# Kernel optimization log

Hardware: AMD Instinct MI355X
Metric: run time of the kernel (lower is better)

Reference implementation:

```python
import jax, jax.numpy as jnp
import numpy as np

N, T, S, E, H, DFF = 4, 2048, 2048, 512, 8, 2048
DH = E // H
EPS = 1e-5


def layer_norm(x, w, b):
    m = jnp.mean(x, axis=-1, keepdims=True)
    v = jnp.mean(jnp.square(x - m), axis=-1, keepdims=True)
    return (x - m) * jax.lax.rsqrt(v + EPS) * w + b


def mha(q, k, v, wq, bq, wk, bk, wv, bv, wo, bo, mask=None):
    # q: (N,Tq,E), k/v: (N,Tk,E); torch Linear convention: y = x @ W.T + b
    Nq, Tq, _ = q.shape
    Tk = k.shape[1]
    Q = (q @ wq.T + bq).reshape(Nq, Tq, H, DH).transpose(0, 2, 1, 3)  # (N,H,Tq,DH)
    K = (k @ wk.T + bk).reshape(Nq, Tk, H, DH).transpose(0, 2, 1, 3)
    V = (v @ wv.T + bv).reshape(Nq, Tk, H, DH).transpose(0, 2, 1, 3)
    scores = jnp.einsum('bhtd,bhsd->bhts', Q, K) * (1.0 / np.sqrt(DH))  # (N,H,Tq,Tk)
    if mask is not None:
        scores = jnp.where(mask, scores, jnp.float32(-1e9))
    attn = jax.nn.softmax(scores, axis=-1)
    out = jnp.einsum('bhts,bhsd->bhtd', attn, V)  # (N,H,Tq,DH)
    out = out.transpose(0, 2, 1, 3).reshape(Nq, Tq, E)
    return out @ wo.T + bo


def setup_inputs() -> dict:
    key = jax.random.key(0)
    ks = jax.random.split(key, 20)
    s = 0.02

    def lin(k, out_d, in_d):
        return jax.random.normal(k, (out_d, in_d), jnp.float32) * s

    inp = {
        'tgt': jax.random.normal(ks[0], (N, T, E), jnp.float32),
        'memory': jax.random.normal(ks[1], (N, S, E), jnp.float32),
        'tgt_mask': jnp.tril(jnp.ones((T, T), dtype=bool)),  # causal (T,T)
        # self-attention params
        'sa_wq': lin(ks[2], E, E), 'sa_bq': jnp.zeros((E,), jnp.float32),
        'sa_wk': lin(ks[3], E, E), 'sa_bk': jnp.zeros((E,), jnp.float32),
        'sa_wv': lin(ks[4], E, E), 'sa_bv': jnp.zeros((E,), jnp.float32),
        'sa_wo': lin(ks[5], E, E), 'sa_bo': jnp.zeros((E,), jnp.float32),
        # cross-attention params
        'ca_wq': lin(ks[6], E, E), 'ca_bq': jnp.zeros((E,), jnp.float32),
        'ca_wk': lin(ks[7], E, E), 'ca_bk': jnp.zeros((E,), jnp.float32),
        'ca_wv': lin(ks[8], E, E), 'ca_bv': jnp.zeros((E,), jnp.float32),
        'ca_wo': lin(ks[9], E, E), 'ca_bo': jnp.zeros((E,), jnp.float32),
        # FFN params
        'w1': lin(ks[10], DFF, E), 'b1': jnp.zeros((DFF,), jnp.float32),
        'w2': lin(ks[11], E, DFF), 'b2': jnp.zeros((E,), jnp.float32),
        # LayerNorm params
        'ln1_w': jnp.ones((E,), jnp.float32), 'ln1_b': jnp.zeros((E,), jnp.float32),
        'ln2_w': jnp.ones((E,), jnp.float32), 'ln2_b': jnp.zeros((E,), jnp.float32),
        'ln3_w': jnp.ones((E,), jnp.float32), 'ln3_b': jnp.zeros((E,), jnp.float32),
    }
    return inp


def reference(tgt, memory, tgt_mask,
              sa_wq, sa_bq, sa_wk, sa_bk, sa_wv, sa_bv, sa_wo, sa_bo,
              ca_wq, ca_bq, ca_wk, ca_bk, ca_wv, ca_bv, ca_wo, ca_bo,
              w1, b1, w2, b2,
              ln1_w, ln1_b, ln2_w, ln2_b, ln3_w, ln3_b):
    # stage 1: masked self-attention + residual + LN (dropout=0 / eval mode)
    sa = mha(tgt, tgt, tgt, sa_wq, sa_bq, sa_wk, sa_bk, sa_wv, sa_bv, sa_wo, sa_bo, mask=tgt_mask)
    x = layer_norm(tgt + sa, ln1_w, ln1_b)
    # stage 2: cross-attention over encoder memory + residual + LN
    ca = mha(x, memory, memory, ca_wq, ca_bq, ca_wk, ca_bk, ca_wv, ca_bv, ca_wo, ca_bo)
    x = layer_norm(x + ca, ln2_w, ln2_b)
    # stage 3: FFN (ReLU) + residual + LN
    mlp = jax.nn.relu(x @ w1.T + b1) @ w2.T + b2
    out = layer_norm(x + mlp, ln3_w, ln3_b)
    return out
```

## Files before the change

### kernel.cpp

```cpp
#include <hip/hip_runtime.h>
#include <hip/hip_bf16.h>
#include <cstdint>

typedef short short8 __attribute__((ext_vector_type(8)));
typedef short short4v __attribute__((ext_vector_type(4)));
typedef float f32x4 __attribute__((ext_vector_type(4)));
typedef float f32x16 __attribute__((ext_vector_type(16)));

#define GLL16(gp, lp) __builtin_amdgcn_global_load_lds( \
    (const __attribute__((address_space(1))) unsigned int*)(gp), \
    (__attribute__((address_space(3))) unsigned int*)(lp), 16, 0, 0)
#define WAITV(n) asm volatile("s_waitcnt vmcnt(" #n ")" ::: "memory")

__device__ __forceinline__ float bf2f(ushort u) {
    union { unsigned int i; float f; } v; v.i = ((unsigned int)u) << 16; return v.f;
}
__device__ __forceinline__ ushort f2bf(float f) {
    union { float f; unsigned int u; } v; v.f = f;
    unsigned int r = v.u + 0x7FFFu + ((v.u >> 16) & 1u);
    return (ushort)(r >> 16);
}
__device__ __forceinline__ int cvtpk_bf16(float lo, float hi) {
    int r;
    asm("v_cvt_pk_bf16_f32 %0, %1, %2" : "=v"(r) : "v"(lo), "v"(hi));
    return r;
}
__device__ __forceinline__ void plane32_swap(int& a, int& b) {
    asm volatile("v_permlane32_swap_b32 %0, %1" : "+v"(a), "+v"(b));
}
__device__ __forceinline__ float fast_exp2(float x) {
    float r;
    asm("v_exp_f32 %0, %1" : "=v"(r) : "v"(x));
    return r;
}

#define SCQ 0.18033688f

struct CvtArgs {
    const float* src[12];
    ushort*      dst[12];
};
__global__ __launch_bounds__(256) void f2b_all(CvtArgs a)
{
    int id = blockIdx.x;
    int seg, boff;
    if (id < 4096)       { seg = 0; boff = id; }
    else if (id < 8192)  { seg = 1; boff = id - 4096; }
    else if (id < 10240) { int t = id - 8192; seg = 2 + (t >> 8); boff = t & 255; }
    else if (id < 11264) { seg = 10; boff = id - 10240; }
    else                 { seg = 11; boff = id - 11264; }
    int i = (boff * 256 + threadIdx.x) * 4;
    f32x4 v = *(const f32x4*)(a.src[seg] + i);
    short4v o;
#pragma unroll
    for (int e = 0; e < 4; ++e) o[e] = (short)f2bf(v[e]);
    *(short4v*)(a.dst[seg] + i) = o;
}

template<int MODE, int DEPTH, int TN>
__global__ __launch_bounds__(256) void gemm_bt(
    const ushort* __restrict__ A, const ushort* __restrict__ W,
    const float* __restrict__ b0, const float* __restrict__ b1,
    const float* __restrict__ b2,
    ushort* __restrict__ C0, ushort* __restrict__ C1, ushort* __restrict__ C2,
    int M, int N, int K)
{
    constexpr int NI = TN / 32;
    constexpr int L  = (TN == 128) ? 4 : 3;
    __shared__ ushort As[DEPTH][128 * 32];
    __shared__ ushort Bs[DEPTH][TN * 32];
    const int tid = threadIdx.x;
    const int l  = tid & 63;
    const int w  = tid >> 6;
    const int wr = w >> 1, wc = w & 1;
    const int bn = blockIdx.x, bm = blockIdx.y;
    const int lg = l >> 4, li = l & 15;

    const ushort* Ab = A + (size_t)(bm * 128) * K;
    const ushort* Bb = W + (size_t)(bn * TN) * K;

    f32x4 acc[4][NI] = {};

    const int r0 = tid >> 2,         s0 = (tid & 3) ^ ((r0 >> 2) & 3);
    const int r1 = (tid + 256) >> 2, s1 = (tid & 3) ^ ((r1 >> 2) & 3);

    auto stage = [&](int buf, int kt) {
        const ushort* Ak = Ab + kt * 32;
        const ushort* Bk = Bb + kt * 32;
        GLL16(Ak + (size_t)r0 * K + s0 * 8, &As[buf][tid * 8]);
        GLL16(Ak + (size_t)r1 * K + s1 * 8, &As[buf][(tid + 256) * 8]);
        GLL16(Bk + (size_t)r0 * K + s0 * 8, &Bs[buf][tid * 8]);
        if (TN == 128)
            GLL16(Bk + (size_t)r1 * K + s1 * 8, &Bs[buf][(tid + 256) * 8]);
    };

    const int nk = K >> 5;
#pragma unroll
    for (int p = 0; p < DEPTH - 1; ++p)
        if (p < nk) stage(p, p);

    for (int kt = 0; kt < nk; ++kt) {
        const int b = kt & (DEPTH - 1);
        const int nxt = kt + DEPTH - 1;
        if (nxt < nk) stage(nxt & (DEPTH - 1), nxt);
        const int rem = nk - 1 - kt;
        const int fl = rem < DEPTH - 1 ? rem : DEPTH - 1;
        if (L == 4) {
            if (fl >= 3)      WAITV(12);
            else if (fl == 2) WAITV(8);
            else if (fl == 1) WAITV(4);
            else              WAITV(0);
        } else {
            if (fl >= 3)      WAITV(9);
            else if (fl == 2) WAITV(6);
            else if (fl == 1) WAITV(3);
            else              WAITV(0);
        }
        __builtin_amdgcn_s_barrier();
        __builtin_amdgcn_sched_barrier(0);

        short8 af[4], bfr[NI];
#pragma unroll
        for (int mi = 0; mi < 4; ++mi) {
            int row = wr * 64 + mi * 16 + li;
            int ch  = lg ^ ((row >> 2) & 3);
            af[mi] = *(const short8*)(&As[b][row * 32 + ch * 8]);
        }
#pragma unroll
        for (int ni = 0; ni < NI; ++ni) {
            int row = wc * (TN / 2) + ni * 16 + li;
            int ch  = lg ^ ((row >> 2) & 3);
            bfr[ni] = *(const short8*)(&Bs[b][row * 32 + ch * 8]);
        }
#pragma unroll
        for (int mi = 0; mi < 4; ++mi)
#pragma unroll
            for (int ni = 0; ni < NI; ++ni)
                acc[mi][ni] = __builtin_amdgcn_mfma_f32_16x16x32_bf16(
                    af[mi], bfr[ni], acc[mi][ni], 0, 0, 0);

        __builtin_amdgcn_sched_barrier(0);
        asm volatile("s_waitcnt lgkmcnt(0)" ::: "memory");
        __builtin_amdgcn_s_barrier();
    }

    const int crow0 = bm * 128 + wr * 64 + lg * 4;
    const int ccol0 = bn * TN + wc * (TN / 2) + li;
    const int sec = (MODE == 2 || MODE == 3) ? (bn >> 2) : 0;
    const float* bp = b0;
    ushort* Cw = C0;
    bool vsec = false;
    if (MODE == 2) {
        bp = (sec == 0) ? b0 : (sec == 1) ? b1 : b2;
        Cw = (sec == 0) ? C0 : (sec == 1) ? C1 : C2;
        vsec = (sec == 2);
    } else if (MODE == 3) {
        bp = (sec == 0) ? b0 : b1;
        Cw = (sec == 0) ? C0 : C1;
        vsec = (sec == 1);
    }
    const int Nout = (MODE == 2 || MODE == 3) ? 512 : N;
    const float scl = (MODE == 4 || (MODE == 2 && sec == 0)) ? SCQ : 1.f;

#pragma unroll
    for (int ni = 0; ni < NI; ++ni) {
        int col = ccol0 + ni * 16;
        int cl  = (MODE == 2 || MODE == 3) ? (col & 511) : col;
        float bv = bp[cl];
#pragma unroll
        for (int mi = 0; mi < 4; ++mi) {
            int row = crow0 + mi * 16;
            if (vsec) {
                int n = row >> 11, t = row & 2047;
                int h = cl >> 6,  d = cl & 63;
                size_t base = ((size_t)((n * 8 + h) * 64 + d)) * 2048 + t;
                short4v pk;
#pragma unroll
                for (int r = 0; r < 4; ++r) pk[r] = (short)f2bf(acc[mi][ni][r] + bv);
                *(short4v*)(Cw + base) = pk;
            } else {
#pragma unroll
                for (int r = 0; r < 4; ++r) {
                    float v = (acc[mi][ni][r] + bv) * scl;
                    if (MODE == 1) v = fmaxf(v, 0.f);
                    Cw[(size_t)(row + r) * Nout + cl] = f2bf(v);
                }
            }
        }
    }
}

template<bool CAUSAL>
__global__ __launch_bounds__(256) void attn_kernel(
    const ushort* __restrict__ Q, const ushort* __restrict__ K,
    const ushort* __restrict__ Vt, ushort* __restrict__ P0,
    ushort* __restrict__ P1, float* __restrict__ Ls, int Tk)
{
    __shared__ ushort SH[16384];
    const int tid = threadIdx.x;
    const int l = tid & 63, wq = tid >> 6;
    const int c = l & 31, hi = l >> 5;

    int qt, nh, ck;
    if (CAUSAL) {
        int g = (int)blockIdx.x >> 6;
        qt = (g < 8) ? (15 - g) : (g - 8);
        int r = blockIdx.x & 63;
        nh = r >> 1; ck = r & 1;
    } else {
        int pos = ((int)blockIdx.x & 7) * 128 + ((int)blockIdx.x >> 3);
        nh = pos >> 5; ck = (pos >> 4) & 1; qt = pos & 15;
    }
    const int q0 = qt * 128;
    const int n = nh >> 3, h = nh & 7;
    const int qrow = q0 + wq * 32 + c;

    short8 qf[4];
#pragma unroll
    for (int s = 0; s < 4; ++s)
        qf[s] = *(const short8*)(Q + (size_t)(n * 2048 + qrow) * 512
                                   + h * 64 + s * 16 + hi * 8);

    f32x16 oacc[2] = {};
    f32x16 oS = {};
    const short ONE = (short)0x3F80;
    const short8 ones = {ONE, ONE, ONE, ONE, ONE, ONE, ONE, ONE};

    const ushort* Kbase = K + (size_t)(n * 2048) * 512 + h * 64;
    const ushort* Vbase = Vt + (size_t)nh * 64 * Tk;

    const int rowA = tid >> 3;
    const int csA  = (tid & 7) ^ (rowA & 7);

    auto stage = [&](int buf, int j0) {
        ushort* kd = SH + buf * 4096;
        ushort* vd = SH + 8192 + buf * 4096;
        GLL16(Kbase + (size_t)(j0 + rowA) * 512 + csA * 8,      kd + tid * 8);
        GLL16(Kbase + (size_t)(j0 + rowA + 32) * 512 + csA * 8, kd + (tid + 256) * 8);
        GLL16(Vbase + (size_t)rowA * Tk + j0 + csA * 8,         vd + tid * 8);
        GLL16(Vbase + (size_t)(rowA + 32) * Tk + j0 + csA * 8,  vd + (tid + 256) * 8);
    };

    const int cnt = CAUSAL ? (qt + 1) : (Tk >> 7);

    stage(0, ck * 64);
    for (int s = 0; s < cnt; ++s) {
        const int b  = s & 1;
        const int j0 = (ck + 2 * s) << 6;
        if (s + 1 < cnt) {
            stage(b ^ 1, j0 + 128);
            WAITV(4);
        } else {
            WAITV(0);
        }
        __builtin_amdgcn_s_barrier();
        __builtin_amdgcn_sched_barrier(0);

        const ushort* kls = SH + b * 4096;
        const ushort* vls = SH + 8192 + b * 4096;

        f32x16 sacc[2] = {};
        __builtin_amdgcn_s_setprio(1);
#pragma unroll
        for (int ks = 0; ks < 4; ++ks) {
#pragma unroll
            for (int t2 = 0; t2 < 2; ++t2) {
                int row = t2 * 32 + c;
                int ch  = (ks * 2 + hi) ^ (row & 7);
                short8 kf = *(const short8*)(kls + row * 64 + ch * 8);
                sacc[t2] = __builtin_amdgcn_mfma_f32_32x32x16_bf16(
                    kf, qf[ks], sacc[t2], 0, 0, 0);
            }
        }
        __builtin_amdgcn_s_setprio(0);

        const bool domask = CAUSAL && (j0 + 64 > q0);
#pragma unroll
        for (int t2 = 0; t2 < 2; ++t2) {
            float pv[16];
#pragma unroll
            for (int reg = 0; reg < 16; ++reg) {
                float p = fast_exp2(sacc[t2][reg]);
                if (domask) {
                    int jg = j0 + t2 * 32 + (reg & 3) + 8 * (reg >> 2) + 4 * hi;
                    if (jg > qrow) p = 0.f;
                }
                pv[reg] = p;
            }
            int X0 = cvtpk_bf16(pv[0],  pv[1]),  Y0 = cvtpk_bf16(pv[2],  pv[3]);
            int X1 = cvtpk_bf16(pv[4],  pv[5]),  Y1 = cvtpk_bf16(pv[6],  pv[7]);
            int X2 = cvtpk_bf16(pv[8],  pv[9]),  Y2 = cvtpk_bf16(pv[10], pv[11]);
            int X3 = cvtpk_bf16(pv[12], pv[13]), Y3 = cvtpk_bf16(pv[14], pv[15]);
            plane32_swap(X0, X1); plane32_swap(Y0, Y1);
            plane32_swap(X2, X3); plane32_swap(Y2, Y3);
            union { int i[4]; short8 s; } pa0 = {{X0, Y0, X1, Y1}},
                                          pa1 = {{X2, Y2, X3, Y3}};
            __builtin_amdgcn_s_setprio(1);
            oS = __builtin_amdgcn_mfma_f32_32x32x16_bf16(pa0.s, ones, oS, 0, 0, 0);
            oS = __builtin_amdgcn_mfma_f32_32x32x16_bf16(pa1.s, ones, oS, 0, 0, 0);
#pragma unroll
            for (int sp = 0; sp < 2; ++sp) {
                short8 pa = sp ? pa1.s : pa0.s;
#pragma unroll
                for (int dc = 0; dc < 2; ++dc) {
                    int row = dc * 32 + c;
                    int ch  = (t2 * 4 + sp * 2 + hi) ^ (row & 7);
                    short8 vb = *(const short8*)(vls + row * 64 + ch * 8);
                    oacc[dc] = __builtin_amdgcn_mfma_f32_32x32x16_bf16(
                        pa, vb, oacc[dc], 0, 0, 0);
                }
            }
            __builtin_amdgcn_s_setprio(0);
        }

        __builtin_amdgcn_sched_barrier(0);
        asm volatile("s_waitcnt lgkmcnt(0)" ::: "memory");
        __builtin_amdgcn_s_barrier();
    }

    ushort* Pw = ck ? P1 : P0;
    if (c == 0) {
#pragma unroll
        for (int reg = 0; reg < 16; ++reg) {
            int qloc = (reg & 3) + 8 * (reg >> 2) + 4 * hi;
            Ls[ck * 65536 + nh * 2048 + q0 + wq * 32 + qloc] = oS[reg];
        }
    }
#pragma unroll
    for (int dc = 0; dc < 2; ++dc)
#pragma unroll
        for (int reg = 0; reg < 16; ++reg) {
            int qloc = (reg & 3) + 8 * (reg >> 2) + 4 * hi;
            size_t off = (size_t)(n * 2048 + q0 + wq * 32 + qloc) * 512
                       + h * 64 + dc * 32 + c;
            Pw[off] = f2bf(oacc[dc][reg]);
        }
}

__global__ __launch_bounds__(256) void attn_merge(
    const ushort* __restrict__ P0, const ushort* __restrict__ P1,
    const float* __restrict__ Ls, ushort* __restrict__ out)
{
    const int row = blockIdx.x * 4 + (threadIdx.x >> 6);
    const int l = threadIdx.x & 63;
    const size_t off = (size_t)row * 512 + l * 8;
    const int n = row >> 11, q = row & 2047, h = l >> 3;
    const int lidx = (n * 8 + h) * 2048 + q;
    float linv = 1.f / (Ls[lidx] + Ls[65536 + lidx]);
    short8 a = *(const short8*)(P0 + off);
    short8 b = *(const short8*)(P1 + off);
    short8 o;
#pragma unroll
    for (int e = 0; e < 8; ++e)
        o[e] = (short)f2bf((bf2f((ushort)a[e]) + bf2f((ushort)b[e])) * linv);
    *(short8*)(out + off) = o;
}

template<int F32OUT>
__global__ __launch_bounds__(256) void ln_kernel(
    const ushort* __restrict__ X, const ushort* __restrict__ Y,
    const float* __restrict__ W, const float* __restrict__ B,
    void* __restrict__ outp)
{
    const int row = blockIdx.x * 4 + (threadIdx.x >> 6);
    const int l = threadIdx.x & 63;
    const size_t off = (size_t)row * 512 + l * 8;
    short8 xv = *(const short8*)(X + off);
    short8 yv = *(const short8*)(Y + off);
    float v[8], s = 0.f, s2 = 0.f;
#pragma unroll
    for (int e = 0; e < 8; ++e) {
        float f = bf2f((ushort)xv[e]) + bf2f((ushort)yv[e]);
        v[e] = f; s += f; s2 += f * f;
    }
#pragma unroll
    for (int m = 1; m < 64; m <<= 1) {
        s  += __shfl_xor(s,  m);
        s2 += __shfl_xor(s2, m);
    }
    float mean = s * (1.f / 512.f);
    float var  = s2 * (1.f / 512.f) - mean * mean;
    float rs   = rsqrtf(var + 1e-5f);
    f32x4 w0 = *(const f32x4*)(W + l * 8);
    f32x4 w1 = *(const f32x4*)(W + l * 8 + 4);
    f32x4 b0 = *(const f32x4*)(B + l * 8);
    f32x4 b1 = *(const f32x4*)(B + l * 8 + 4);
    float wv[8] = {w0[0], w0[1], w0[2], w0[3], w1[0], w1[1], w1[2], w1[3]};
    float bv[8] = {b0[0], b0[1], b0[2], b0[3], b1[0], b1[1], b1[2], b1[3]};
    if (F32OUT) {
        float* out = (float*)outp;
#pragma unroll
        for (int e = 0; e < 8; ++e)
            out[off + e] = (v[e] - mean) * rs * wv[e] + bv[e];
    } else {
        ushort* out = (ushort*)outp;
        short8 ov;
#pragma unroll
        for (int e = 0; e < 8; ++e)
            ov[e] = (short)f2bf((v[e] - mean) * rs * wv[e] + bv[e]);
        *(short8*)(out + off) = ov;
    }
}

extern "C" void kernel_launch(void* const* d_in, const int* in_sizes, int n_in,
                              void* d_out, int out_size, void* d_ws, size_t ws_size,
                              hipStream_t stream)
{
    (void)in_sizes; (void)n_in; (void)out_size; (void)ws_size;
    const float* tgt  = (const float*)d_in[0];
    const float* mem  = (const float*)d_in[1];
    const float* sa_wq = (const float*)d_in[3];
    const float* sa_bq = (const float*)d_in[4];
    const float* sa_wk = (const float*)d_in[5];
    const float* sa_bk = (const float*)d_in[6];
    const float* sa_wv = (const float*)d_in[7];
    const float* sa_bv = (const float*)d_in[8];
    const float* sa_wo = (const float*)d_in[9];
    const float* sa_bo = (const float*)d_in[10];
    const float* ca_wq = (const float*)d_in[11];
    const float* ca_bq = (const float*)d_in[12];
    const float* ca_wk = (const float*)d_in[13];
    const float* ca_bk = (const float*)d_in[14];
    const float* ca_wv = (const float*)d_in[15];
    const float* ca_bv = (const float*)d_in[16];
    const float* ca_wo = (const float*)d_in[17];
    const float* ca_bo = (const float*)d_in[18];
    const float* w1    = (const float*)d_in[19];
    const float* b1    = (const float*)d_in[20];
    const float* w2    = (const float*)d_in[21];
    const float* b2    = (const float*)d_in[22];
    const float* ln1w  = (const float*)d_in[23];
    const float* ln1b  = (const float*)d_in[24];
    const float* ln2w  = (const float*)d_in[25];
    const float* ln2b  = (const float*)d_in[26];
    const float* ln3w  = (const float*)d_in[27];
    const float* ln3b  = (const float*)d_in[28];

    const size_t SE = (size_t)8192 * 512;
    const size_t EE = (size_t)512 * 512;
    ushort* ws = (ushort*)d_ws;
    ushort* Wb   = ws;
    ushort* bsqkv = Wb;
    ushort* bswo  = Wb + 3 * EE;
    ushort* bcwq  = Wb + 4 * EE;
    ushort* bckv  = Wb + 5 * EE;
    ushort* bcwo  = Wb + 7 * EE;
    ushort* bw1   = Wb + 8 * EE;
    ushort* bw2   = bw1 + 4 * EE;
    ushort* tgtb = Wb + 16 * EE;
    ushort* memb = tgtb + SE;
    ushort* Qb   = memb + SE;
    ushort* Kb   = Qb + SE;
    ushort* Vb   = Kb + SE;
    ushort* X1   = Vb + SE;
    ushort* AO   = X1 + SE;
    float*  LsBuf = (float*)(AO + SE);
    ushort* PO   = Qb;
    ushort* X2   = tgtb;
    ushort* Hb   = Qb;

    dim3 blk(256);
    dim3 gqkv(12, 64);
    dim3 gkv(8, 64);
    dim3 g64n(8, 64);
    dim3 g2048(16, 64);
    dim3 ga(1024);
    dim3 gln(2048);

    CvtArgs ca;
    ca.src[0] = tgt;    ca.dst[0] = tgtb;
    ca.src[1] = mem;    ca.dst[1] = memb;
    ca.src[2] = sa_wq;  ca.dst[2] = bsqkv;
    ca.src[3] = sa_wk;  ca.dst[3] = bsqkv + EE;
    ca.src[4] = sa_wv;  ca.dst[4] = bsqkv + 2 * EE;
    ca.src[5] = sa_wo;  ca.dst[5] = bswo;
    ca.src[6] = ca_wq;  ca.dst[6] = bcwq;
    ca.src[7] = ca_wk;  ca.dst[7] = bckv;
    ca.src[8] = ca_wv;  ca.dst[8] = bckv + EE;
    ca.src[9] = ca_wo;  ca.dst[9] = bcwo;
    ca.src[10] = w1;    ca.dst[10] = bw1;
    ca.src[11] = w2;    ca.dst[11] = bw2;
    f2b_all<<<12288, blk, 0, stream>>>(ca);

    gemm_bt<2, 2, 128><<<gqkv, blk, 0, stream>>>(tgtb, bsqkv, sa_bq, sa_bk, sa_bv,
                                                 Qb, Kb, Vb, 8192, 1536, 512);
    attn_kernel<true><<<ga, blk, 0, stream>>>(Qb, Kb, Vb, AO, X1, LsBuf, 2048);
    attn_merge<<<gln, blk, 0, stream>>>(AO, X1, LsBuf, AO);
    gemm_bt<0, 4, 64><<<g64n, blk, 0, stream>>>(AO, bswo, sa_bo, nullptr, nullptr,
                                                PO, nullptr, nullptr, 8192, 512, 512);
    ln_kernel<0><<<gln, blk, 0, stream>>>(tgtb, PO, ln1w, ln1b, X1);

    gemm_bt<4, 4, 64><<<g64n, blk, 0, stream>>>(X1, bcwq, ca_bq, nullptr, nullptr,
                                                Qb, nullptr, nullptr, 8192, 512, 512);
    gemm_bt<3, 2, 128><<<gkv, blk, 0, stream>>>(memb, bckv, ca_bk, ca_bv, nullptr,
                                                Kb, Vb, nullptr, 8192, 1024, 512);
    attn_kernel<false><<<ga, blk, 0, stream>>>(Qb, Kb, Vb, AO, tgtb, LsBuf, 2048);
    attn_merge<<<gln, blk, 0, stream>>>(AO, tgtb, LsBuf, AO);
    gemm_bt<0, 4, 64><<<g64n, blk, 0, stream>>>(AO, bcwo, ca_bo, nullptr, nullptr,
                                                PO, nullptr, nullptr, 8192, 512, 512);
    ln_kernel<0><<<gln, blk, 0, stream>>>(X1, PO, ln2w, ln2b, X2);

    gemm_bt<1, 2, 128><<<g2048, blk, 0, stream>>>(X2, bw1, b1, nullptr, nullptr,
                                                  Hb, nullptr, nullptr, 8192, 2048, 512);
    gemm_bt<0, 4, 64><<<g64n, blk, 0, stream>>>(Hb, bw2, b2, nullptr, nullptr,
                                                AO, nullptr, nullptr, 8192, 512, 2048);
    ln_kernel<1><<<gln, blk, 0, stream>>>(X2, AO, ln3w, ln3b, d_out);
}
```

Measured before the change: 284.8 us.

## Double attention query tile per block to 256 rows, halving K/V staging

Each attention block now handles 256 query rows (64 per wave, split into two 32-row chunks) instead of 128. Each K/V tile staged into LDS is reused across twice as many queries, and the grid shrinks from 1024 to 512 blocks. In the causal case, waves skip key tiles that lie entirely beyond their rows. The cost is more registers per wave (two sets of accumulators and Q fragments), fewer blocks in flight, and more causal imbalance since waves in one block finish at different points.

Result: slower. 302.4 us (+6.2%).

```diff
diff --git a/kernel.cpp b/kernel.cpp
--- a/kernel.cpp
+++ b/kernel.cpp
@@ -204,25 +204,27 @@
     int qt, nh, ck;
     if (CAUSAL) {
         int g = (int)blockIdx.x >> 6;
-        qt = (g < 8) ? (15 - g) : (g - 8);
+        qt = (g < 4) ? (7 - g) : (g - 4);
         int r = blockIdx.x & 63;
         nh = r >> 1; ck = r & 1;
     } else {
-        int pos = ((int)blockIdx.x & 7) * 128 + ((int)blockIdx.x >> 3);
-        nh = pos >> 5; ck = (pos >> 4) & 1; qt = pos & 15;
-    }
-    const int q0 = qt * 128;
+        int pos = ((int)blockIdx.x & 7) * 64 + ((int)blockIdx.x >> 3);
+        nh = pos >> 4; ck = (pos >> 3) & 1; qt = pos & 7;
+    }
+    const int q0 = qt * 256;
     const int n = nh >> 3, h = nh & 7;
-    const int qrow = q0 + wq * 32 + c;
-
-    short8 qf[4];
-#pragma unroll
-    for (int s = 0; s < 4; ++s)
-        qf[s] = *(const short8*)(Q + (size_t)(n * 2048 + qrow) * 512
-                                   + h * 64 + s * 16 + hi * 8);
-
-    f32x16 oacc[2] = {};
-    f32x16 oS = {};
+    const int qw = q0 + wq * 64;
+
+    short8 qf[2][4];
+#pragma unroll
+    for (int ic = 0; ic < 2; ++ic)
+#pragma unroll
+        for (int s = 0; s < 4; ++s)
+            qf[ic][s] = *(const short8*)(Q + (size_t)(n * 2048 + qw + ic * 32 + c) * 512
+                                           + h * 64 + s * 16 + hi * 8);
+
+    f32x16 oacc[2][2] = {};
+    f32x16 oS[2] = {};
     const short ONE = (short)0x3F80;
     const short8 ones = {ONE, ONE, ONE, ONE, ONE, ONE, ONE, ONE};
 
@@ -241,7 +243,7 @@
         GLL16(Vbase + (size_t)(rowA + 32) * Tk + j0 + csA * 8,  vd + (tid + 256) * 8);
     };
 
-    const int cnt = CAUSAL ? (qt + 1) : (Tk >> 7);
+    const int cnt = CAUSAL ? 2 * (qt + 1) : (Tk >> 7);
 
     stage(0, ck * 64);
     for (int s = 0; s < cnt; ++s) {
@@ -256,61 +258,74 @@
         __builtin_amdgcn_s_barrier();
         __builtin_amdgcn_sched_barrier(0);
 
-        const ushort* kls = SH + b * 4096;
-        const ushort* vls = SH + 8192 + b * 4096;
-
-        f32x16 sacc[2] = {};
-        __builtin_amdgcn_s_setprio(1);
-#pragma unroll
-        for (int ks = 0; ks < 4; ++ks) {
+        const bool active = !CAUSAL || (j0 < qw + 64);
+        if (active) {
+            const ushort* kls = SH + b * 4096;
+            const ushort* vls = SH + 8192 + b * 4096;
+            const bool domask = CAUSAL && (j0 + 64 > qw);
+
 #pragma unroll
             for (int t2 = 0; t2 < 2; ++t2) {
-                int row = t2 * 32 + c;
-                int ch  = (ks * 2 + hi) ^ (row & 7);
-                short8 kf = *(const short8*)(kls + row * 64 + ch * 8);
-                sacc[t2] = __builtin_amdgcn_mfma_f32_32x32x16_bf16(
-                    kf, qf[ks], sacc[t2], 0, 0, 0);
+                f32x16 sacc[2] = {};
+                __builtin_amdgcn_s_setprio(1);
+#pragma unroll
+                for (int ks = 0; ks < 4; ++ks) {
+                    int row = t2 * 32 + c;
+                    int ch  = (ks * 2 + hi) ^ (row & 7);
+                    short8 kf = *(const short8*)(kls + row * 64 + ch * 8);
+                    sacc[0] = __builtin_amdgcn_mfma_f32_32x32x16_bf16(
+                        kf, qf[0][ks], sacc[0], 0, 0, 0);
+                    sacc[1] = __builtin_amdgcn_mfma_f32_32x32x16_bf16(
+                        kf, qf[1][ks], sacc[1], 0, 0, 0);
+                }
+                __builtin_amdgcn_s_setprio(0);
+
+                short8 pa[2][2];
+#pragma unroll
+                for (int ic = 0; ic < 2; ++ic) {
+                    const int qrow = qw + ic * 32 + c;
+                    float pv[16];
+#pragma unroll
+                    for (int reg = 0; reg < 16; ++reg) {
+                        float p = fast_exp2(sacc[ic][reg]);
+                        if (domask) {
+                            int jg = j0 + t2 * 32 + (reg & 3) + 8 * (reg >> 2) + 4 * hi;
+                            if (jg > qrow) p = 0.f;
+                        }
+                        pv[reg] = p;
+                    }
+                    int X0 = cvtpk_bf16(pv[0],  pv[1]),  Y0 = cvtpk_bf16(pv[2],  pv[3]);
+                    int X1 = cvtpk_bf16(pv[4],  pv[5]),  Y1 = cvtpk_bf16(pv[6],  pv[7]);
+                    int X2 = cvtpk_bf16(pv[8],  pv[9]),  Y2 = cvtpk_bf16(pv[10], pv[11]);
+                    int X3 = cvtpk_bf16(pv[12], pv[13]), Y3 = cvtpk_bf16(pv[14], pv[15]);
+                    plane32_swap(X0, X1); plane32_swap(Y0, Y1);
+                    plane32_swap(X2, X3); plane32_swap(Y2, Y3);
+                    union { int i[4]; short8 s; } u0 = {{X0, Y0, X1, Y1}},
+                                                  u1 = {{X2, Y2, X3, Y3}};
+                    pa[ic][0] = u0.s;
+                    pa[ic][1] = u1.s;
+                }
+
+                __builtin_amdgcn_s_setprio(1);
+                oS[0] = __builtin_amdgcn_mfma_f32_32x32x16_bf16(pa[0][0], ones, oS[0], 0, 0, 0);
+                oS[0] = __builtin_amdgcn_mfma_f32_32x32x16_bf16(pa[0][1], ones, oS[0], 0, 0, 0);
+                oS[1] = __builtin_amdgcn_mfma_f32_32x32x16_bf16(pa[1][0], ones, oS[1], 0, 0, 0);
+                oS[1] = __builtin_amdgcn_mfma_f32_32x32x16_bf16(pa[1][1], ones, oS[1], 0, 0, 0);
+#pragma unroll
+                for (int sp = 0; sp < 2; ++sp) {
+#pragma unroll
+                    for (int dc = 0; dc < 2; ++dc) {
+                        int row = dc * 32 + c;
+                        int ch  = (t2 * 4 + sp * 2 + hi) ^ (row & 7);
+                        short8 vb = *(const short8*)(vls + row * 64 + ch * 8);
+                        oacc[0][dc] = __builtin_amdgcn_mfma_f32_32x32x16_bf16(
+                            pa[0][sp], vb, oacc[0][dc], 0, 0, 0);
+                        oacc[1][dc] = __builtin_amdgcn_mfma_f32_32x32x16_bf16(
+                            pa[1][sp], vb, oacc[1][dc], 0, 0, 0);
+                    }
+                }
+                __builtin_amdgcn_s_setprio(0);
             }
-        }
-        __builtin_amdgcn_s_setprio(0);
-
-        const bool domask = CAUSAL && (j0 + 64 > q0);
-#pragma unroll
-        for (int t2 = 0; t2 < 2; ++t2) {
-            float pv[16];
-#pragma unroll
-            for (int reg = 0; reg < 16; ++reg) {
-                float p = fast_exp2(sacc[t2][reg]);
-                if (domask) {
-                    int jg = j0 + t2 * 32 + (reg & 3) + 8 * (reg >> 2) + 4 * hi;
-                    if (jg > qrow) p = 0.f;
-                }
-                pv[reg] = p;
-            }
-            int X0 = cvtpk_bf16(pv[0],  pv[1]),  Y0 = cvtpk_bf16(pv[2],  pv[3]);
-            int X1 = cvtpk_bf16(pv[4],  pv[5]),  Y1 = cvtpk_bf16(pv[6],  pv[7]);
-            int X2 = cvtpk_bf16(pv[8],  pv[9]),  Y2 = cvtpk_bf16(pv[10], pv[11]);
-            int X3 = cvtpk_bf16(pv[12], pv[13]), Y3 = cvtpk_bf16(pv[14], pv[15]);
-            plane32_swap(X0, X1); plane32_swap(Y0, Y1);
-            plane32_swap(X2, X3); plane32_swap(Y2, Y3);
-            union { int i[4]; short8 s; } pa0 = {{X0, Y0, X1, Y1}},
-                                          pa1 = {{X2, Y2, X3, Y3}};
-            __builtin_amdgcn_s_setprio(1);
-            oS = __builtin_amdgcn_mfma_f32_32x32x16_bf16(pa0.s, ones, oS, 0, 0, 0);
-            oS = __builtin_amdgcn_mfma_f32_32x32x16_bf16(pa1.s, ones, oS, 0, 0, 0);
-#pragma unroll
-            for (int sp = 0; sp < 2; ++sp) {
-                short8 pa = sp ? pa1.s : pa0.s;
-#pragma unroll
-                for (int dc = 0; dc < 2; ++dc) {
-                    int row = dc * 32 + c;
-                    int ch  = (t2 * 4 + sp * 2 + hi) ^ (row & 7);
-                    short8 vb = *(const short8*)(vls + row * 64 + ch * 8);
-                    oacc[dc] = __builtin_amdgcn_mfma_f32_32x32x16_bf16(
-                        pa, vb, oacc[dc], 0, 0, 0);
-                }
-            }
-            __builtin_amdgcn_s_setprio(0);
         }
 
         __builtin_amdgcn_sched_barrier(0);
@@ -321,20 +336,24 @@
     ushort* Pw = ck ? P1 : P0;
     if (c == 0) {
 #pragma unroll
-        for (int reg = 0; reg < 16; ++reg) {
-            int qloc = (reg & 3) + 8 * (reg >> 2) + 4 * hi;
-            Ls[ck * 65536 + nh * 2048 + q0 + wq * 32 + qloc] = oS[reg];
-        }
-    }
-#pragma unroll
-    for (int dc = 0; dc < 2; ++dc)
-#pragma unroll
-        for (int reg = 0; reg < 16; ++reg) {
-            int qloc = (reg & 3) + 8 * (reg >> 2) + 4 * hi;
-            size_t off = (size_t)(n * 2048 + q0 + wq * 32 + qloc) * 512
-                       + h * 64 + dc * 32 + c;
-            Pw[off] = f2bf(oacc[dc][reg]);
-        }
+        for (int ic = 0; ic < 2; ++ic)
+#pragma unroll
+            for (int reg = 0; reg < 16; ++reg) {
+                int qloc = (reg & 3) + 8 * (reg >> 2) + 4 * hi;
+                Ls[ck * 65536 + nh * 2048 + qw + ic * 32 + qloc] = oS[ic][reg];
+            }
+    }
+#pragma unroll
+    for (int ic = 0; ic < 2; ++ic)
+#pragma unroll
+        for (int dc = 0; dc < 2; ++dc)
+#pragma unroll
+            for (int reg = 0; reg < 16; ++reg) {
+                int qloc = (reg & 3) + 8 * (reg >> 2) + 4 * hi;
+                size_t off = (size_t)(n * 2048 + qw + ic * 32 + qloc) * 512
+                           + h * 64 + dc * 32 + c;
+                Pw[off] = f2bf(oacc[ic][dc][reg]);
+            }
 }
 
 __global__ __launch_bounds__(256) void attn_merge(
@@ -464,7 +483,7 @@
     dim3 gkv(8, 64);
     dim3 g64n(8, 64);
     dim3 g2048(16, 64);
-    dim3 ga(1024);
+    dim3 ga(512);
     dim3 gln(2048);
 
     CvtArgs ca;
```

## Split attention key dimension four ways and skip fully masked key tiles per wave

Applied to the files above, without the earlier changes.

The attention kernel now splits each query tile's key range into four interleaved chunks instead of two, doubling the grid to 2048 blocks. Each block writes its own partial output and row-sum buffer, and the merge kernel combines four partials. Within causal tiles, waves whose query rows lie entirely before a key block skip that block's compute, cutting wasted masked work. The cost is more partial-output memory traffic in the merge, an extra workspace region, and a shorter per-block loop that pipelines less.

Result: slower. 298.3 us (+4.7%).

```diff
diff --git a/kernel.cpp b/kernel.cpp
--- a/kernel.cpp
+++ b/kernel.cpp
@@ -194,7 +194,8 @@
 __global__ __launch_bounds__(256) void attn_kernel(
     const ushort* __restrict__ Q, const ushort* __restrict__ K,
     const ushort* __restrict__ Vt, ushort* __restrict__ P0,
-    ushort* __restrict__ P1, float* __restrict__ Ls, int Tk)
+    ushort* __restrict__ P1, ushort* __restrict__ P2, ushort* __restrict__ P3,
+    float* __restrict__ Ls, int Tk)
 {
     __shared__ ushort SH[16384];
     const int tid = threadIdx.x;
@@ -203,17 +204,18 @@
 
     int qt, nh, ck;
     if (CAUSAL) {
-        int g = (int)blockIdx.x >> 6;
+        int g = (int)blockIdx.x >> 7;
         qt = (g < 8) ? (15 - g) : (g - 8);
-        int r = blockIdx.x & 63;
-        nh = r >> 1; ck = r & 1;
+        int r = blockIdx.x & 127;
+        nh = r >> 2; ck = r & 3;
     } else {
-        int pos = ((int)blockIdx.x & 7) * 128 + ((int)blockIdx.x >> 3);
-        nh = pos >> 5; ck = (pos >> 4) & 1; qt = pos & 15;
+        int pos = ((int)blockIdx.x & 7) * 256 + ((int)blockIdx.x >> 3);
+        nh = pos >> 6; ck = (pos >> 4) & 3; qt = pos & 15;
     }
     const int q0 = qt * 128;
     const int n = nh >> 3, h = nh & 7;
-    const int qrow = q0 + wq * 32 + c;
+    const int qw = q0 + wq * 32;
+    const int qrow = qw + c;
 
     short8 qf[4];
 #pragma unroll
@@ -241,14 +243,14 @@
         GLL16(Vbase + (size_t)(rowA + 32) * Tk + j0 + csA * 8,  vd + (tid + 256) * 8);
     };
 
-    const int cnt = CAUSAL ? (qt + 1) : (Tk >> 7);
-
-    stage(0, ck * 64);
+    const int cnt = CAUSAL ? ((2 * qt + 5 - ck) >> 2) : (Tk >> 8);
+
+    if (cnt > 0) stage(0, ck * 64);
     for (int s = 0; s < cnt; ++s) {
         const int b  = s & 1;
-        const int j0 = (ck + 2 * s) << 6;
+        const int j0 = (ck + 4 * s) << 6;
         if (s + 1 < cnt) {
-            stage(b ^ 1, j0 + 128);
+            stage(b ^ 1, j0 + 256);
             WAITV(4);
         } else {
             WAITV(0);
@@ -256,74 +258,78 @@
         __builtin_amdgcn_s_barrier();
         __builtin_amdgcn_sched_barrier(0);
 
-        const ushort* kls = SH + b * 4096;
-        const ushort* vls = SH + 8192 + b * 4096;
-
-        f32x16 sacc[2] = {};
-        __builtin_amdgcn_s_setprio(1);
-#pragma unroll
-        for (int ks = 0; ks < 4; ++ks) {
-#pragma unroll
-            for (int t2 = 0; t2 < 2; ++t2) {
-                int row = t2 * 32 + c;
-                int ch  = (ks * 2 + hi) ^ (row & 7);
-                short8 kf = *(const short8*)(kls + row * 64 + ch * 8);
-                sacc[t2] = __builtin_amdgcn_mfma_f32_32x32x16_bf16(
-                    kf, qf[ks], sacc[t2], 0, 0, 0);
-            }
-        }
-        __builtin_amdgcn_s_setprio(0);
-
-        const bool domask = CAUSAL && (j0 + 64 > q0);
-#pragma unroll
-        for (int t2 = 0; t2 < 2; ++t2) {
-            float pv[16];
-#pragma unroll
-            for (int reg = 0; reg < 16; ++reg) {
-                float p = fast_exp2(sacc[t2][reg]);
-                if (domask) {
-                    int jg = j0 + t2 * 32 + (reg & 3) + 8 * (reg >> 2) + 4 * hi;
-                    if (jg > qrow) p = 0.f;
-                }
-                pv[reg] = p;
-            }
-            int X0 = cvtpk_bf16(pv[0],  pv[1]),  Y0 = cvtpk_bf16(pv[2],  pv[3]);
-            int X1 = cvtpk_bf16(pv[4],  pv[5]),  Y1 = cvtpk_bf16(pv[6],  pv[7]);
-            int X2 = cvtpk_bf16(pv[8],  pv[9]),  Y2 = cvtpk_bf16(pv[10], pv[11]);
-            int X3 = cvtpk_bf16(pv[12], pv[13]), Y3 = cvtpk_bf16(pv[14], pv[15]);
-            plane32_swap(X0, X1); plane32_swap(Y0, Y1);
-            plane32_swap(X2, X3); plane32_swap(Y2, Y3);
-            union { int i[4]; short8 s; } pa0 = {{X0, Y0, X1, Y1}},
-                                          pa1 = {{X2, Y2, X3, Y3}};
+        const bool active = !CAUSAL || (j0 < qw + 32);
+        if (active) {
+            const ushort* kls = SH + b * 4096;
+            const ushort* vls = SH + 8192 + b * 4096;
+            const bool domask = CAUSAL && (j0 + 64 > qw);
+
+            f32x16 sacc[2] = {};
             __builtin_amdgcn_s_setprio(1);
-            oS = __builtin_amdgcn_mfma_f32_32x32x16_bf16(pa0.s, ones, oS, 0, 0, 0);
-            oS = __builtin_amdgcn_mfma_f32_32x32x16_bf16(pa1.s, ones, oS, 0, 0, 0);
-#pragma unroll
-            for (int sp = 0; sp < 2; ++sp) {
-                short8 pa = sp ? pa1.s : pa0.s;
-#pragma unroll
-                for (int dc = 0; dc < 2; ++dc) {
-                    int row = dc * 32 + c;
-                    int ch  = (t2 * 4 + sp * 2 + hi) ^ (row & 7);
-                    short8 vb = *(const short8*)(vls + row * 64 + ch * 8);
-                    oacc[dc] = __builtin_amdgcn_mfma_f32_32x32x16_bf16(
-                        pa, vb, oacc[dc], 0, 0, 0);
+#pragma unroll
+            for (int ks = 0; ks < 4; ++ks) {
+#pragma unroll
+                for (int t2 = 0; t2 < 2; ++t2) {
+                    int row = t2 * 32 + c;
+                    int ch  = (ks * 2 + hi) ^ (row & 7);
+                    short8 kf = *(const short8*)(kls + row * 64 + ch * 8);
+                    sacc[t2] = __builtin_amdgcn_mfma_f32_32x32x16_bf16(
+                        kf, qf[ks], sacc[t2], 0, 0, 0);
                 }
             }
             __builtin_amdgcn_s_setprio(0);
+
+#pragma unroll
+            for (int t2 = 0; t2 < 2; ++t2) {
+                float pv[16];
+#pragma unroll
+                for (int reg = 0; reg < 16; ++reg) {
+                    float p = fast_exp2(sacc[t2][reg]);
+                    if (domask) {
+                        int jg = j0 + t2 * 32 + (reg & 3) + 8 * (reg >> 2) + 4 * hi;
+                        if (jg > qrow) p = 0.f;
+                    }
+                    pv[reg] = p;
+                }
+                int X0 = cvtpk_bf16(pv[0],  pv[1]),  Y0 = cvtpk_bf16(pv[2],  pv[3]);
+                int X1 = cvtpk_bf16(pv[4],  pv[5]),  Y1 = cvtpk_bf16(pv[6],  pv[7]);
+                int X2 = cvtpk_bf16(pv[8],  pv[9]),  Y2 = cvtpk_bf16(pv[10], pv[11]);
+                int X3 = cvtpk_bf16(pv[12], pv[13]), Y3 = cvtpk_bf16(pv[14], pv[15]);
+                plane32_swap(X0, X1); plane32_swap(Y0, Y1);
+                plane32_swap(X2, X3); plane32_swap(Y2, Y3);
+                union { int i[4]; short8 s; } pa0 = {{X0, Y0, X1, Y1}},
+                                              pa1 = {{X2, Y2, X3, Y3}};
+                __builtin_amdgcn_s_setprio(1);
+                oS = __builtin_amdgcn_mfma_f32_32x32x16_bf16(pa0.s, ones, oS, 0, 0, 0);
+                oS = __builtin_amdgcn_mfma_f32_32x32x16_bf16(pa1.s, ones, oS, 0, 0, 0);
+#pragma unroll
+                for (int sp = 0; sp < 2; ++sp) {
+                    short8 pa = sp ? pa1.s : pa0.s;
+#pragma unroll
+                    for (int dc = 0; dc < 2; ++dc) {
+                        int row = dc * 32 + c;
+                        int ch  = (t2 * 4 + sp * 2 + hi) ^ (row & 7);
+                        short8 vb = *(const short8*)(vls + row * 64 + ch * 8);
+                        oacc[dc] = __builtin_amdgcn_mfma_f32_32x32x16_bf16(
+                            pa, vb, oacc[dc], 0, 0, 0);
+                    }
+                }
+                __builtin_amdgcn_s_setprio(0);
+            }
         }
 
         __builtin_amdgcn_sched_barrier(0);
         asm volatile("s_waitcnt lgkmcnt(0)" ::: "memory");
         __builtin_amdgcn_s_barrier();
     }
-
-    ushort* Pw = ck ? P1 : P0;
+    WAITV(0);
+
+    ushort* Pw = (ck == 0) ? P0 : (ck == 1) ? P1 : (ck == 2) ? P2 : P3;
     if (c == 0) {
 #pragma unroll
         for (int reg = 0; reg < 16; ++reg) {
             int qloc = (reg & 3) + 8 * (reg >> 2) + 4 * hi;
-            Ls[ck * 65536 + nh * 2048 + q0 + wq * 32 + qloc] = oS[reg];
+            Ls[ck * 65536 + nh * 2048 + qw + qloc] = oS[reg];
         }
     }
 #pragma unroll
@@ -331,7 +337,7 @@
 #pragma unroll
         for (int reg = 0; reg < 16; ++reg) {
             int qloc = (reg & 3) + 8 * (reg >> 2) + 4 * hi;
-            size_t off = (size_t)(n * 2048 + q0 + wq * 32 + qloc) * 512
+            size_t off = (size_t)(n * 2048 + qw + qloc) * 512
                        + h * 64 + dc * 32 + c;
             Pw[off] = f2bf(oacc[dc][reg]);
         }
@@ -339,6 +345,7 @@
 
 __global__ __launch_bounds__(256) void attn_merge(
     const ushort* __restrict__ P0, const ushort* __restrict__ P1,
+    const ushort* __restrict__ P2, const ushort* __restrict__ P3,
     const float* __restrict__ Ls, ushort* __restrict__ out)
 {
     const int row = blockIdx.x * 4 + (threadIdx.x >> 6);
@@ -346,13 +353,19 @@
     const size_t off = (size_t)row * 512 + l * 8;
     const int n = row >> 11, q = row & 2047, h = l >> 3;
     const int lidx = (n * 8 + h) * 2048 + q;
-    float linv = 1.f / (Ls[lidx] + Ls[65536 + lidx]);
+    float linv = 1.f / (Ls[lidx] + Ls[65536 + lidx]
+                      + Ls[131072 + lidx] + Ls[196608 + lidx]);
     short8 a = *(const short8*)(P0 + off);
     short8 b = *(const short8*)(P1 + off);
+    short8 cc = *(const short8*)(P2 + off);
+    short8 d = *(const short8*)(P3 + off);
     short8 o;
 #pragma unroll
-    for (int e = 0; e < 8; ++e)
-        o[e] = (short)f2bf((bf2f((ushort)a[e]) + bf2f((ushort)b[e])) * linv);
+    for (int e = 0; e < 8; ++e) {
+        float s = bf2f((ushort)a[e]) + bf2f((ushort)b[e])
+                + bf2f((ushort)cc[e]) + bf2f((ushort)d[e]);
+        o[e] = (short)f2bf(s * linv);
+    }
     *(short8*)(out + off) = o;
 }
 
@@ -455,6 +468,8 @@
     ushort* X1   = Vb + SE;
     ushort* AO   = X1 + SE;
     float*  LsBuf = (float*)(AO + SE);
+    ushort* P2   = (ushort*)(LsBuf + 4 * 65536);
+    ushort* P3   = P2 + SE;
     ushort* PO   = Qb;
     ushort* X2   = tgtb;
     ushort* Hb   = Qb;
@@ -464,7 +479,7 @@
     dim3 gkv(8, 64);
     dim3 g64n(8, 64);
     dim3 g2048(16, 64);
-    dim3 ga(1024);
+    dim3 ga(2048);
     dim3 gln(2048);
 
     CvtArgs ca;
@@ -484,8 +499,9 @@
 
     gemm_bt<2, 2, 128><<<gqkv, blk, 0, stream>>>(tgtb, bsqkv, sa_bq, sa_bk, sa_bv,
                                                  Qb, Kb, Vb, 8192, 1536, 512);
-    attn_kernel<true><<<ga, blk, 0, stream>>>(Qb, Kb, Vb, AO, X1, LsBuf, 2048);
-    attn_merge<<<gln, blk, 0, stream>>>(AO, X1, LsBuf, AO);
+    attn_kernel<true><<<ga, blk, 0, stream>>>(Qb, Kb, Vb, AO, X1, P2, P3,
+                                              LsBuf, 2048);
+    attn_merge<<<gln, blk, 0, stream>>>(AO, X1, P2, P3, LsBuf, AO);
     gemm_bt<0, 4, 64><<<g64n, blk, 0, stream>>>(AO, bswo, sa_bo, nullptr, nullptr,
                                                 PO, nullptr, nullptr, 8192, 512, 512);
     ln_kernel<0><<<gln, blk, 0, stream>>>(tgtb, PO, ln1w, ln1b, X1);
@@ -494,8 +510,9 @@
                                                 Qb, nullptr, nullptr, 8192, 512, 512);
     gemm_bt<3, 2, 128><<<gkv, blk, 0, stream>>>(memb, bckv, ca_bk, ca_bv, nullptr,
                                                 Kb, Vb, nullptr, 8192, 1024, 512);
-    attn_kernel<false><<<ga, blk, 0, stream>>>(Qb, Kb, Vb, AO, tgtb, LsBuf, 2048);
-    attn_merge<<<gln, blk, 0, stream>>>(AO, tgtb, LsBuf, AO);
+    attn_kernel<false><<<ga, blk, 0, stream>>>(Qb, Kb, Vb, AO, tgtb, P2, P3,
+                                               LsBuf, 2048);
+    attn_merge<<<gln, blk, 0, stream>>>(AO, tgtb, P2, P3, LsBuf, AO);
     gemm_bt<0, 4, 64><<<g64n, blk, 0, stream>>>(AO, bcwo, ca_bo, nullptr, nullptr,
                                                 PO, nullptr, nullptr, 8192, 512, 512);
     ln_kernel<0><<<gln, blk, 0, stream>>>(X1, PO, ln2w, ln2b, X2);
```

## Split KV range contiguously, skip fully masked wave tiles, rotate LDS swizzle

Applied to the files above, without the earlier changes.

The two key-chunk halves are now contiguous ranges of 64-wide KV tiles split evenly, instead of interleaved 64-tile strides. This balances causal work between the two splits. Each wave skips the QK/PV compute for tiles entirely above its 32-row causal band, and the mask check is narrowed to per-wave rows. The LDS swizzle adds a row-group rotation to reduce bank conflicts in the K/V fragment reads. A trailing vmcnt wait is added for safety. The risk is wave divergence at barriers, and skipped waves still wait on the shared loads.

Result: slower. 295.6 us, median of 2 (+3.8%).

```diff
diff --git a/kernel.cpp b/kernel.cpp
--- a/kernel.cpp
+++ b/kernel.cpp
@@ -213,7 +213,8 @@
     }
     const int q0 = qt * 128;
     const int n = nh >> 3, h = nh & 7;
-    const int qrow = q0 + wq * 32 + c;
+    const int qw = q0 + wq * 32;
+    const int qrow = qw + c;
 
     short8 qf[4];
 #pragma unroll
@@ -230,25 +231,28 @@
     const ushort* Vbase = Vt + (size_t)nh * 64 * Tk;
 
     const int rowA = tid >> 3;
-    const int csA  = (tid & 7) ^ (rowA & 7);
+    const int cs0 = (((tid & 7) - (rowA >> 3)) & 7) ^ (rowA & 7);
+    const int cs1 = (((tid & 7) - (rowA >> 3) + 4) & 7) ^ (rowA & 7);
 
     auto stage = [&](int buf, int j0) {
         ushort* kd = SH + buf * 4096;
         ushort* vd = SH + 8192 + buf * 4096;
-        GLL16(Kbase + (size_t)(j0 + rowA) * 512 + csA * 8,      kd + tid * 8);
-        GLL16(Kbase + (size_t)(j0 + rowA + 32) * 512 + csA * 8, kd + (tid + 256) * 8);
-        GLL16(Vbase + (size_t)rowA * Tk + j0 + csA * 8,         vd + tid * 8);
-        GLL16(Vbase + (size_t)(rowA + 32) * Tk + j0 + csA * 8,  vd + (tid + 256) * 8);
+        GLL16(Kbase + (size_t)(j0 + rowA) * 512 + cs0 * 8,      kd + tid * 8);
+        GLL16(Kbase + (size_t)(j0 + rowA + 32) * 512 + cs1 * 8, kd + (tid + 256) * 8);
+        GLL16(Vbase + (size_t)rowA * Tk + j0 + cs0 * 8,         vd + tid * 8);
+        GLL16(Vbase + (size_t)(rowA + 32) * Tk + j0 + cs1 * 8,  vd + (tid + 256) * 8);
     };
 
-    const int cnt = CAUSAL ? (qt + 1) : (Tk >> 7);
-
-    stage(0, ck * 64);
+    const int total = CAUSAL ? (2 * qt + 2) : (Tk >> 6);
+    const int start = (ck * total) >> 1;
+    const int cnt   = (((ck + 1) * total) >> 1) - start;
+
+    if (cnt > 0) stage(0, start << 6);
     for (int s = 0; s < cnt; ++s) {
         const int b  = s & 1;
-        const int j0 = (ck + 2 * s) << 6;
+        const int j0 = (start + s) << 6;
         if (s + 1 < cnt) {
-            stage(b ^ 1, j0 + 128);
+            stage(b ^ 1, j0 + 64);
             WAITV(4);
         } else {
             WAITV(0);
@@ -256,74 +260,78 @@
         __builtin_amdgcn_s_barrier();
         __builtin_amdgcn_sched_barrier(0);
 
-        const ushort* kls = SH + b * 4096;
-        const ushort* vls = SH + 8192 + b * 4096;
-
-        f32x16 sacc[2] = {};
-        __builtin_amdgcn_s_setprio(1);
-#pragma unroll
-        for (int ks = 0; ks < 4; ++ks) {
-#pragma unroll
-            for (int t2 = 0; t2 < 2; ++t2) {
-                int row = t2 * 32 + c;
-                int ch  = (ks * 2 + hi) ^ (row & 7);
-                short8 kf = *(const short8*)(kls + row * 64 + ch * 8);
-                sacc[t2] = __builtin_amdgcn_mfma_f32_32x32x16_bf16(
-                    kf, qf[ks], sacc[t2], 0, 0, 0);
-            }
-        }
-        __builtin_amdgcn_s_setprio(0);
-
-        const bool domask = CAUSAL && (j0 + 64 > q0);
-#pragma unroll
-        for (int t2 = 0; t2 < 2; ++t2) {
-            float pv[16];
-#pragma unroll
-            for (int reg = 0; reg < 16; ++reg) {
-                float p = fast_exp2(sacc[t2][reg]);
-                if (domask) {
-                    int jg = j0 + t2 * 32 + (reg & 3) + 8 * (reg >> 2) + 4 * hi;
-                    if (jg > qrow) p = 0.f;
-                }
-                pv[reg] = p;
-            }
-            int X0 = cvtpk_bf16(pv[0],  pv[1]),  Y0 = cvtpk_bf16(pv[2],  pv[3]);
-            int X1 = cvtpk_bf16(pv[4],  pv[5]),  Y1 = cvtpk_bf16(pv[6],  pv[7]);
-            int X2 = cvtpk_bf16(pv[8],  pv[9]),  Y2 = cvtpk_bf16(pv[10], pv[11]);
-            int X3 = cvtpk_bf16(pv[12], pv[13]), Y3 = cvtpk_bf16(pv[14], pv[15]);
-            plane32_swap(X0, X1); plane32_swap(Y0, Y1);
-            plane32_swap(X2, X3); plane32_swap(Y2, Y3);
-            union { int i[4]; short8 s; } pa0 = {{X0, Y0, X1, Y1}},
-                                          pa1 = {{X2, Y2, X3, Y3}};
+        const bool active = !CAUSAL || (j0 < qw + 32);
+        if (active) {
+            const ushort* kls = SH + b * 4096;
+            const ushort* vls = SH + 8192 + b * 4096;
+            const bool domask = CAUSAL && (j0 + 64 > qw);
+
+            f32x16 sacc[2] = {};
             __builtin_amdgcn_s_setprio(1);
-            oS = __builtin_amdgcn_mfma_f32_32x32x16_bf16(pa0.s, ones, oS, 0, 0, 0);
-            oS = __builtin_amdgcn_mfma_f32_32x32x16_bf16(pa1.s, ones, oS, 0, 0, 0);
-#pragma unroll
-            for (int sp = 0; sp < 2; ++sp) {
-                short8 pa = sp ? pa1.s : pa0.s;
-#pragma unroll
-                for (int dc = 0; dc < 2; ++dc) {
-                    int row = dc * 32 + c;
-                    int ch  = (t2 * 4 + sp * 2 + hi) ^ (row & 7);
-                    short8 vb = *(const short8*)(vls + row * 64 + ch * 8);
-                    oacc[dc] = __builtin_amdgcn_mfma_f32_32x32x16_bf16(
-                        pa, vb, oacc[dc], 0, 0, 0);
+#pragma unroll
+            for (int ks = 0; ks < 4; ++ks) {
+#pragma unroll
+                for (int t2 = 0; t2 < 2; ++t2) {
+                    int row = t2 * 32 + c;
+                    int ch  = (((ks * 2 + hi) ^ (row & 7)) + (row >> 3)) & 7;
+                    short8 kf = *(const short8*)(kls + row * 64 + ch * 8);
+                    sacc[t2] = __builtin_amdgcn_mfma_f32_32x32x16_bf16(
+                        kf, qf[ks], sacc[t2], 0, 0, 0);
                 }
             }
             __builtin_amdgcn_s_setprio(0);
+
+#pragma unroll
+            for (int t2 = 0; t2 < 2; ++t2) {
+                float pv[16];
+#pragma unroll
+                for (int reg = 0; reg < 16; ++reg) {
+                    float p = fast_exp2(sacc[t2][reg]);
+                    if (domask) {
+                        int jg = j0 + t2 * 32 + (reg & 3) + 8 * (reg >> 2) + 4 * hi;
+                        if (jg > qrow) p = 0.f;
+                    }
+                    pv[reg] = p;
+                }
+                int X0 = cvtpk_bf16(pv[0],  pv[1]),  Y0 = cvtpk_bf16(pv[2],  pv[3]);
+                int X1 = cvtpk_bf16(pv[4],  pv[5]),  Y1 = cvtpk_bf16(pv[6],  pv[7]);
+                int X2 = cvtpk_bf16(pv[8],  pv[9]),  Y2 = cvtpk_bf16(pv[10], pv[11]);
+                int X3 = cvtpk_bf16(pv[12], pv[13]), Y3 = cvtpk_bf16(pv[14], pv[15]);
+                plane32_swap(X0, X1); plane32_swap(Y0, Y1);
+                plane32_swap(X2, X3); plane32_swap(Y2, Y3);
+                union { int i[4]; short8 s; } pa0 = {{X0, Y0, X1, Y1}},
+                                              pa1 = {{X2, Y2, X3, Y3}};
+                __builtin_amdgcn_s_setprio(1);
+                oS = __builtin_amdgcn_mfma_f32_32x32x16_bf16(pa0.s, ones, oS, 0, 0, 0);
+                oS = __builtin_amdgcn_mfma_f32_32x32x16_bf16(pa1.s, ones, oS, 0, 0, 0);
+#pragma unroll
+                for (int sp = 0; sp < 2; ++sp) {
+                    short8 pa = sp ? pa1.s : pa0.s;
+#pragma unroll
+                    for (int dc = 0; dc < 2; ++dc) {
+                        int row = dc * 32 + c;
+                        int ch  = (((t2 * 4 + sp * 2 + hi) ^ (row & 7)) + (row >> 3)) & 7;
+                        short8 vb = *(const short8*)(vls + row * 64 + ch * 8);
+                        oacc[dc] = __builtin_amdgcn_mfma_f32_32x32x16_bf16(
+                            pa, vb, oacc[dc], 0, 0, 0);
+                    }
+                }
+                __builtin_amdgcn_s_setprio(0);
+            }
         }
 
         __builtin_amdgcn_sched_barrier(0);
         asm volatile("s_waitcnt lgkmcnt(0)" ::: "memory");
         __builtin_amdgcn_s_barrier();
     }
+    WAITV(0);
 
     ushort* Pw = ck ? P1 : P0;
     if (c == 0) {
 #pragma unroll
         for (int reg = 0; reg < 16; ++reg) {
             int qloc = (reg & 3) + 8 * (reg >> 2) + 4 * hi;
-            Ls[ck * 65536 + nh * 2048 + q0 + wq * 32 + qloc] = oS[reg];
+            Ls[ck * 65536 + nh * 2048 + qw + qloc] = oS[reg];
         }
     }
 #pragma unroll
@@ -331,7 +339,7 @@
 #pragma unroll
         for (int reg = 0; reg < 16; ++reg) {
             int qloc = (reg & 3) + 8 * (reg >> 2) + 4 * hi;
-            size_t off = (size_t)(n * 2048 + q0 + wq * 32 + qloc) * 512
+            size_t off = (size_t)(n * 2048 + qw + qloc) * 512
                        + h * 64 + dc * 32 + c;
             Pw[off] = f2bf(oacc[dc][reg]);
         }
```
